# Kernel optimization log

Measured on AMD Instinct MI355X. Metric: run time of the kernel, lower is better.

Reference implementation:

```python
import jax, jax.numpy as jnp
import numpy as np

B, S, D, H = 4, 2048, 1024, 16
DH = D // H          # per-head attention size (attention_size // n_heads)
F = 4 * D            # FFN hidden
EPS = 1e-5


def _layer_norm(x, g, b):
    m = jnp.mean(x, axis=-1, keepdims=True)
    v = jnp.mean(jnp.square(x - m), axis=-1, keepdims=True)
    return (x - m) * jax.lax.rsqrt(v + EPS) * g + b


def setup_inputs() -> dict:
    key = jax.random.key(0)
    ks = jax.random.split(key, 12)
    s = 0.02
    x = jax.random.normal(ks[0], (B, S, D), dtype=jnp.float32)
    # causal mask: True = masked (strict upper triangle)
    mask = jnp.broadcast_to(jnp.triu(jnp.ones((S, S), dtype=bool), k=1), (B, S, S))
    wq = jax.random.normal(ks[1], (H, D, DH), dtype=jnp.float32) * s
    wk = jax.random.normal(ks[2], (H, D, DH), dtype=jnp.float32) * s
    wv = jax.random.normal(ks[3], (H, D, DH), dtype=jnp.float32) * s
    wo = jax.random.normal(ks[4], (D, D), dtype=jnp.float32) * s   # attention_size -> embedding_dim
    w1 = jax.random.normal(ks[5], (D, F), dtype=jnp.float32) * s
    b1 = jax.random.normal(ks[6], (F,), dtype=jnp.float32) * s
    w2 = jax.random.normal(ks[7], (F, D), dtype=jnp.float32) * s
    b2 = jax.random.normal(ks[8], (D,), dtype=jnp.float32) * s
    ln1_g = jnp.ones((D,), jnp.float32) + jax.random.normal(ks[9], (D,), jnp.float32) * s
    ln1_b = jax.random.normal(ks[10], (D,), jnp.float32) * s
    ln2_g = jnp.ones((D,), jnp.float32) + jax.random.normal(ks[11], (D,), jnp.float32) * s
    ln2_b = jnp.zeros((D,), jnp.float32)
    return {"x": x, "mask": mask, "wq": wq, "wk": wk, "wv": wv, "wo": wo,
            "w1": w1, "b1": b1, "w2": w2, "b2": b2,
            "ln1_g": ln1_g, "ln1_b": ln1_b, "ln2_g": ln2_g, "ln2_b": ln2_b}


def reference(x, mask, wq, wk, wv, wo, w1, b1, w2, b2, ln1_g, ln1_b, ln2_g, ln2_b):
    # --- self-attention block (pre-norm, residual) ---
    h = _layer_norm(x, ln1_g, ln1_b)                       # [B,S,D]
    q = jnp.einsum('bsd,hde->bhse', h, wq)                 # [B,H,S,DH]
    k = jnp.einsum('bsd,hde->bhse', h, wk)
    v = jnp.einsum('bsd,hde->bhse', h, wv)
    scores = jnp.einsum('bhse,bhte->bhst', q, k)           # [B,H,S,S]
    # faithful to source: mask-fill with -inf, THEN divide by sqrt(head_dim)
    scores = jnp.where(mask[:, None, :, :], -jnp.inf, scores) / jnp.sqrt(jnp.float32(DH))
    p = jax.nn.softmax(scores, axis=-1)
    attn = jnp.einsum('bhst,bhte->bhse', p, v)             # [B,H,S,DH]
    concat = attn.transpose(0, 2, 1, 3).reshape(B, S, D)   # heads concatenated on feature dim
    x = x + concat @ wo
    # --- feed-forward block ---
    h2 = _layer_norm(x, ln2_g, ln2_b)
    ff = jax.nn.gelu(h2 @ w1 + b1, approximate=False) @ w2 + b2
    return x + ff
```

## Files before the change

kernel.cpp:

```cpp
#include <hip/hip_runtime.h>
#include <hip/hip_bf16.h>
#include <math.h>


#define Bz 4
#define Sz 2048
#define Dz 1024
#define Hz 16
#define DHz 64
#define Fz 4096
#define Mz 8192

typedef float f32x4 __attribute__((ext_vector_type(4)));
typedef __bf16 bf16x8 __attribute__((ext_vector_type(8)));
typedef __bf16 bf16x4 __attribute__((ext_vector_type(4)));
typedef short s16x4 __attribute__((ext_vector_type(4)));

#define GLOAD_LDS16(g, l)                                                                   \
  __builtin_amdgcn_global_load_lds((const __attribute__((address_space(1))) unsigned int*)(g), \
                                   (__attribute__((address_space(3))) unsigned int*)(l), 16, 0, 0)

static __device__ __forceinline__ unsigned short f2bu(float f) {
  unsigned int u = __float_as_uint(f);
  u += 0x7fffu + ((u >> 16) & 1u);
  return (unsigned short)(u >> 16);
}

static __device__ __forceinline__ f32x4 mfma32(bf16x8 a, bf16x8 b, f32x4 c) {
  return __builtin_amdgcn_mfma_f32_16x16x32_bf16(a, b, c, 0, 0, 0);
}
static __device__ __forceinline__ f32x4 mfma16(s16x4 a, s16x4 b, f32x4 c) {
#if __has_builtin(__builtin_amdgcn_mfma_f32_16x16x16bf16_1k)
  return __builtin_amdgcn_mfma_f32_16x16x16bf16_1k(a, b, c, 0, 0, 0);
#else
  asm("v_mfma_f32_16x16x16_bf16 %0, %1, %2, %0" : "+v"(c) : "v"(a), "v"(b));
  return c;
#endif
}

template <int OFF>
static __device__ __forceinline__ s16x4 tr16(unsigned addr) {
  s16x4 r;
  asm volatile("ds_read_b64_tr_b16 %0, %1 offset:%2" : "=v"(r) : "v"(addr), "i"(OFF));
  return r;
}


__global__ __launch_bounds__(256) void pack_qkv(
    const float* __restrict__ wq, const float* __restrict__ wk, const float* __restrict__ wv,
    unsigned short* __restrict__ outW)
{
  __shared__ float tile[64][65];
  const int blk = blockIdx.x;
  const int dc = blk & 15;
  const int h  = (blk >> 4) & 15;
  const int p  = blk >> 8;
  const float* w = p == 0 ? wq : (p == 1 ? wk : wv);
  const int tid = threadIdx.x;
#pragma unroll
  for (int i = 0; i < 4; ++i) {
    int idx = i * 256 + tid;
    int dl = idx >> 4;
    int e0 = (idx & 15) * 4;
    const float4 v = *(const float4*)&w[(size_t)(h * 1024 + dc * 64 + dl) * 64 + e0];
    tile[dl][e0 + 0] = v.x; tile[dl][e0 + 1] = v.y;
    tile[dl][e0 + 2] = v.z; tile[dl][e0 + 3] = v.w;
  }
  __syncthreads();
#pragma unroll
  for (int i = 0; i < 4; ++i) {
    int idx = i * 256 + tid;
    int e = idx >> 4;
    int d0 = (idx & 15) * 4;
    ushort4 o;
    o.x = f2bu(tile[d0 + 0][e]); o.y = f2bu(tile[d0 + 1][e]);
    o.z = f2bu(tile[d0 + 2][e]); o.w = f2bu(tile[d0 + 3][e]);
    *(ushort4*)&outW[(size_t)(p * 1024 + h * 64 + e) * 1024 + dc * 64 + d0] = o;
  }
}

__global__ __launch_bounds__(256) void transpose_f32_to_bf16(
    const float* __restrict__ in, unsigned short* __restrict__ out, int R, int C)
{
  __shared__ float tile[32][33];
  int c0 = blockIdx.x * 32, r0 = blockIdx.y * 32;
  int x = threadIdx.x, y = threadIdx.y;
#pragma unroll
  for (int i = 0; i < 32; i += 8)
    tile[y + i][x] = in[(size_t)(r0 + y + i) * C + c0 + x];
  __syncthreads();
#pragma unroll
  for (int i = 0; i < 32; i += 8)
    out[(size_t)(c0 + y + i) * R + r0 + x] = f2bu(tile[x][y + i]);
}


__global__ __launch_bounds__(256) void ln_kernel(
    const float* __restrict__ x, const float* __restrict__ gamma, const float* __restrict__ beta,
    unsigned short* __restrict__ outH)
{
  const int row = blockIdx.x;
  const int tid = threadIdx.x;
  const float4 v = ((const float4*)(x + (size_t)row * Dz))[tid];
  float s = v.x + v.y + v.z + v.w;
  float s2 = v.x * v.x + v.y * v.y + v.z * v.z + v.w * v.w;
#pragma unroll
  for (int o = 32; o > 0; o >>= 1) {
    s += __shfl_xor(s, o);
    s2 += __shfl_xor(s2, o);
  }
  __shared__ float ss[4], ss2[4];
  if ((tid & 63) == 0) { ss[tid >> 6] = s; ss2[tid >> 6] = s2; }
  __syncthreads();
  s = ss[0] + ss[1] + ss[2] + ss[3];
  s2 = ss2[0] + ss2[1] + ss2[2] + ss2[3];
  const float mean = s * (1.0f / Dz);
  const float rstd = rsqrtf(s2 * (1.0f / Dz) - mean * mean + 1e-5f);
  const float4 g4 = ((const float4*)gamma)[tid];
  const float4 b4 = ((const float4*)beta)[tid];
  ushort4 o;
  o.x = f2bu((v.x - mean) * rstd * g4.x + b4.x);
  o.y = f2bu((v.y - mean) * rstd * g4.y + b4.y);
  o.z = f2bu((v.z - mean) * rstd * g4.z + b4.z);
  o.w = f2bu((v.w - mean) * rstd * g4.w + b4.w);
  ((ushort4*)(outH + (size_t)row * Dz))[tid] = o;
}


enum { EPI_BF16 = 0, EPI_GELU_BF16 = 1, EPI_RES_F32 = 2, EPI_BIAS_RES_F32 = 3 };

template <int BM, int EPI>
__global__ __launch_bounds__(512, 2) void gemm256(
    const unsigned short* __restrict__ A,
    const unsigned short* __restrict__ BT,
    int M, int N, int K,
    const float* bias, const float* resid,
    unsigned short* outb, float* outf)
{
  constexpr int BN = 256, BK = 32, DEPTH = 4;
  constexpr int ACH = BM / 128;
  constexpr int BCH = 2;
  constexpr int CH = ACH + BCH;
  constexpr int MREP = BM / 32;
  __shared__ unsigned short As[DEPTH][BM * BK];
  __shared__ unsigned short Bs[DEPTH][BN * BK];

  const int tid = threadIdx.x;
  const int lane = tid & 63;
  const int wid = tid >> 6;
  const int wr = wid >> 2;
  const int wc = wid & 3;
  const int rsel = lane & 15;
  const int kgrp = lane >> 4;

  const int nwg = gridDim.x;
  const int bid = blockIdx.x;
  const int id2 = (bid & 7) * (nwg >> 3) + (bid >> 3);
  const int nbx = N / BN;
  const int n0 = (id2 % nbx) * BN;
  const int m0 = (id2 / nbx) * BM;

  f32x4 acc[MREP][4] = {};

  auto issue = [&](int kt, int slot) {
#pragma unroll
    for (int r = 0; r < ACH; ++r) {
      int gc = r * 512 + tid;
      int row = gc >> 2;
      int kcs = (gc & 3) ^ ((row >> 1) & 3);
      GLOAD_LDS16(A + (size_t)(m0 + row) * K + kt * BK + kcs * 8, &As[slot][gc * 8]);
    }
#pragma unroll
    for (int r = 0; r < BCH; ++r) {
      int gc = r * 512 + tid;
      int row = gc >> 2;
      int kcs = (gc & 3) ^ ((row >> 1) & 3);
      GLOAD_LDS16(BT + (size_t)(n0 + row) * K + kt * BK + kcs * 8, &Bs[slot][gc * 8]);
    }
  };

  const int T = K >> 5;
  issue(0, 0); issue(1, 1); issue(2, 2);

  for (int t = 0; t < T; ++t) {
    const int slot = t & 3;
    if (t + 3 < T) issue(t + 3, (t + 3) & 3);
    int rem = T - 1 - t; if (rem > 3) rem = 3;
    if constexpr (CH == 4) {
      if (rem == 3)      asm volatile("s_waitcnt vmcnt(12)" ::: "memory");
      else if (rem == 2) asm volatile("s_waitcnt vmcnt(8)" ::: "memory");
      else if (rem == 1) asm volatile("s_waitcnt vmcnt(4)" ::: "memory");
      else               asm volatile("s_waitcnt vmcnt(0)" ::: "memory");
    } else {
      if (rem == 3)      asm volatile("s_waitcnt vmcnt(9)" ::: "memory");
      else if (rem == 2) asm volatile("s_waitcnt vmcnt(6)" ::: "memory");
      else if (rem == 1) asm volatile("s_waitcnt vmcnt(3)" ::: "memory");
      else               asm volatile("s_waitcnt vmcnt(0)" ::: "memory");
    }
    __builtin_amdgcn_sched_barrier(0);
    __builtin_amdgcn_s_barrier();
    __builtin_amdgcn_sched_barrier(0);

    const unsigned short* Ab = As[slot];
    const unsigned short* Bb = Bs[slot];
    __builtin_amdgcn_s_setprio(1);
    {
      bf16x8 bfr[4], af[MREP];
#pragma unroll
      for (int nf = 0; nf < 4; ++nf) {
        int br = wc * 64 + nf * 16 + rsel;
        bfr[nf] = *(const bf16x8*)&Bb[br * BK + ((kgrp ^ ((br >> 1) & 3)) * 8)];
      }
#pragma unroll
      for (int mf = 0; mf < MREP; ++mf) {
        int ar = wr * (BM / 2) + mf * 16 + rsel;
        af[mf] = *(const bf16x8*)&Ab[ar * BK + ((kgrp ^ ((ar >> 1) & 3)) * 8)];
      }
#pragma unroll
      for (int mf = 0; mf < MREP; ++mf)
#pragma unroll
        for (int nf = 0; nf < 4; ++nf)
          acc[mf][nf] = mfma32(af[mf], bfr[nf], acc[mf][nf]);
    }
    __builtin_amdgcn_s_setprio(0);
    __builtin_amdgcn_sched_barrier(0);
    __builtin_amdgcn_s_barrier();
  }

#pragma unroll
  for (int mf = 0; mf < MREP; ++mf) {
#pragma unroll
    for (int nf = 0; nf < 4; ++nf) {
      const int n = n0 + wc * 64 + nf * 16 + rsel;
#pragma unroll
      for (int j = 0; j < 4; ++j) {
        const int m = m0 + wr * (BM / 2) + mf * 16 + kgrp * 4 + j;
        const size_t idx = (size_t)m * N + n;
        float v = acc[mf][nf][j];
        if constexpr (EPI == EPI_BF16) {
          outb[idx] = f2bu(v);
        } else if constexpr (EPI == EPI_GELU_BF16) {
          v += bias[n];
          v = 0.5f * v * (1.0f + erff(v * 0.70710678118654752f));
          outb[idx] = f2bu(v);
        } else if constexpr (EPI == EPI_RES_F32) {
          outf[idx] = v + resid[idx];
        } else {
          outf[idx] = v + bias[n] + resid[idx];
        }
      }
    }
  }
}


__global__ __launch_bounds__(256, 4) void attn_kernel(
    const unsigned short* __restrict__ QKV,
    unsigned short* __restrict__ outA)
{
  __shared__ unsigned short Kt[64 * 64];
  __shared__ unsigned short Vs[64 * 64];
  const int pi = blockIdx.x;
  const int hh = blockIdx.y;
  const int bb = blockIdx.z;
  const int tid = threadIdx.x;
  const int lane = tid & 63;
  const int w = tid >> 6;
  const int rsel = lane & 15;
  const int kgrp = lane >> 4;
  const int qt[2] = {pi, 31 - pi};

  bf16x8 qf0[2], qf1[2];
  int qg[2];
#pragma unroll
  for (int s = 0; s < 2; ++s) {
    qg[s] = qt[s] * 64 + w * 16 + rsel;
    const size_t rowQ = (size_t)(bb * Sz + qg[s]) * 3072 + hh * 64;
    qf0[s] = *(const bf16x8*)&QKV[rowQ + kgrp * 8];
    qf1[s] = *(const bf16x8*)&QKV[rowQ + 32 + kgrp * 8];
  }

  f32x4 accO[2][4] = {};
  float mr[2] = {-INFINITY, -INFINITY};
  float lr[2] = {0.0f, 0.0f};

  auto vs3 = (__attribute__((address_space(3))) unsigned short*)Vs;
  const unsigned vbase = (unsigned)(uintptr_t)vs3 + (unsigned)lane * 8u;
  constexpr float SCL = 0.18033688011112042f;

  auto proc = [&](const bf16x8& q0, const bf16x8& q1, float& mrun, float& lrun,
                  f32x4* accS, s16x4* pb, bool edge, int qgs, int kb) {
    f32x4 sc[4];
    __builtin_amdgcn_s_setprio(1);
#pragma unroll
    for (int kf = 0; kf < 4; ++kf) {
      int key = kf * 16 + rsel;
      bf16x8 k0 = *(const bf16x8*)&Kt[key * 64 + ((kgrp ^ (key & 7)) * 8)];
      bf16x8 k1 = *(const bf16x8*)&Kt[key * 64 + (((4 + kgrp) ^ (key & 7)) * 8)];
      f32x4 s = {};
      s = mfma32(k0, q0, s);
      s = mfma32(k1, q1, s);
      sc[kf] = s;
    }
    __builtin_amdgcn_s_setprio(0);
    float tmax = -INFINITY;
#pragma unroll
    for (int kf = 0; kf < 4; ++kf)
#pragma unroll
      for (int j = 0; j < 4; ++j) {
        float v = sc[kf][j] * SCL;
        if (edge) {
          int keyg = kb + kf * 16 + kgrp * 4 + j;
          if (keyg > qgs) v = -INFINITY;
        }
        sc[kf][j] = v;
        tmax = fmaxf(tmax, v);
      }
    tmax = fmaxf(tmax, __shfl_xor(tmax, 16));
    tmax = fmaxf(tmax, __shfl_xor(tmax, 32));
    if (!__all(tmax <= mrun + 8.0f)) {
      const float mnew = fmaxf(mrun, tmax);
      const float corr = exp2f(mrun - mnew);
      lrun *= corr;
#pragma unroll
      for (int df = 0; df < 4; ++df) accS[df] *= corr;
      mrun = mnew;
    }
    float psum = 0.0f;
#pragma unroll
    for (int kf = 0; kf < 4; ++kf) {
      bf16x4 pv;
#pragma unroll
      for (int j = 0; j < 4; ++j) {
        float e = exp2f(sc[kf][j] - mrun);
        psum += e;
        pv[j] = (__bf16)e;
      }
      pb[kf] = __builtin_bit_cast(s16x4, pv);
    }
    psum += __shfl_xor(psum, 16);
    psum += __shfl_xor(psum, 32);
    lrun += psum;
  };

  for (int kt = 0; kt <= qt[1]; ++kt) {
    const int kb = kt * 64;
    if (kt) __syncthreads();
#pragma unroll
    for (int r = 0; r < 2; ++r) {
      int c = r * 256 + tid;
      int key = c >> 3;
      int dcs = (c & 7) ^ (key & 7);
      GLOAD_LDS16(QKV + (size_t)(bb * Sz + kb + key) * 3072 + 1024 + hh * 64 + dcs * 8,
                  &Kt[c * 8]);
    }
#pragma unroll
    for (int r = 0; r < 2; ++r) {
      int c = r * 256 + tid;
      int key = ((c >> 3) & 15) * 4 + ((c >> 1) & 3);
      int d = (c >> 7) * 16 + (c & 1) * 8;
      GLOAD_LDS16(QKV + (size_t)(bb * Sz + kb + key) * 3072 + 2048 + hh * 64 + d,
                  &Vs[c * 8]);
    }
    __syncthreads();

    s16x4 pb[2][4];
#pragma unroll
    for (int s = 0; s < 2; ++s)
      if (kt <= qt[s])
        proc(qf0[s], qf1[s], mr[s], lr[s], accO[s], pb[s], kt == qt[s], qg[s], kb);

#pragma unroll
    for (int df = 0; df < 4; ++df) {
      unsigned a = vbase + df * 2048;
      s16x4 vf0 = tr16<0>(a);
      s16x4 vf1 = tr16<512>(a);
      s16x4 vf2 = tr16<1024>(a);
      s16x4 vf3 = tr16<1536>(a);
      asm volatile("s_waitcnt lgkmcnt(0)" ::: "memory");
      __builtin_amdgcn_sched_barrier(0);
      __builtin_amdgcn_s_setprio(1);
#pragma unroll
      for (int s = 0; s < 2; ++s) {
        if (kt <= qt[s]) {
          accO[s][df] = mfma16(vf0, pb[s][0], accO[s][df]);
          accO[s][df] = mfma16(vf1, pb[s][1], accO[s][df]);
          accO[s][df] = mfma16(vf2, pb[s][2], accO[s][df]);
          accO[s][df] = mfma16(vf3, pb[s][3], accO[s][df]);
        }
      }
      __builtin_amdgcn_s_setprio(0);
    }
  }

#pragma unroll
  for (int s = 0; s < 2; ++s) {
    const float rl = 1.0f / lr[s];
    const size_t orow = (size_t)(bb * Sz + qg[s]) * Dz + hh * 64;
#pragma unroll
    for (int df = 0; df < 4; ++df) {
      s16x4 o;
#pragma unroll
      for (int j = 0; j < 4; ++j) o[j] = (short)f2bu(accO[s][df][j] * rl);
      *(s16x4*)&outA[orow + df * 16 + kgrp * 4] = o;
    }
  }
}


extern "C" void kernel_launch(void* const* d_in, const int* in_sizes, int n_in,
                              void* d_out, int out_size, void* d_ws, size_t ws_size,
                              hipStream_t stream) {
  const float* x   = (const float*)d_in[0];
  const float* wq  = (const float*)d_in[2];
  const float* wk  = (const float*)d_in[3];
  const float* wv  = (const float*)d_in[4];
  const float* wo  = (const float*)d_in[5];
  const float* w1  = (const float*)d_in[6];
  const float* b1  = (const float*)d_in[7];
  const float* w2  = (const float*)d_in[8];
  const float* b2  = (const float*)d_in[9];
  const float* g1  = (const float*)d_in[10];
  const float* be1 = (const float*)d_in[11];
  const float* g2  = (const float*)d_in[12];
  const float* be2 = (const float*)d_in[13];
  float* out = (float*)d_out;

  char* ws = (char*)d_ws;
  unsigned short* WqkvT = (unsigned short*)(ws);
  unsigned short* WoT   = (unsigned short*)(ws + 6291456);
  unsigned short* W1T   = (unsigned short*)(ws + 8388608);
  unsigned short* W2T   = (unsigned short*)(ws + 16777216);
  unsigned short* hbuf  = (unsigned short*)(ws + 25165824);
  unsigned short* big   = (unsigned short*)(ws + 41943040);

  dim3 tb(32, 8);
  pack_qkv<<<768, 256, 0, stream>>>(wq, wk, wv, WqkvT);
  transpose_f32_to_bf16<<<dim3(32, 32), tb, 0, stream>>>(wo, WoT, 1024, 1024);
  transpose_f32_to_bf16<<<dim3(128, 32), tb, 0, stream>>>(w1, W1T, 1024, 4096);
  transpose_f32_to_bf16<<<dim3(32, 128), tb, 0, stream>>>(w2, W2T, 4096, 1024);

  ln_kernel<<<Mz, 256, 0, stream>>>(x, g1, be1, hbuf);
  gemm256<128, EPI_BF16><<<768, 512, 0, stream>>>(
      hbuf, WqkvT, Mz, 3072, 1024, nullptr, nullptr, big, nullptr);
  attn_kernel<<<dim3(16, 16, 4), 256, 0, stream>>>(big, hbuf);
  gemm256<128, EPI_RES_F32><<<256, 512, 0, stream>>>(
      hbuf, WoT, Mz, 1024, 1024, nullptr, x, nullptr, out);
  ln_kernel<<<Mz, 256, 0, stream>>>(out, g2, be2, hbuf);
  gemm256<256, EPI_GELU_BF16><<<512, 512, 0, stream>>>(
      hbuf, W1T, Mz, Fz, 1024, b1, nullptr, big, nullptr);
  gemm256<128, EPI_BIAS_RES_F32><<<256, 512, 0, stream>>>(
      big, W2T, Mz, 1024, Fz, b2, out, nullptr, out);
}
```

Before: 497.0 us.

## Replace pipelined 256-wide GEMM with simple single-buffered 128x128 tile GEMM

Swaps the 512-thread, 4-stage multi-buffered GEMM for a 256-thread 128x128 tile kernel. The new kernel loads each K step into shared memory and waits before computing, with no prefetch overlap. The aim is to raise occupancy (3 blocks per CU) and spread work over more blocks, relying on parallelism to hide latency. In exchange it loses the overlap of loads with compute and gets less data reuse per tile.

```diff
diff --git a/kernel.cpp b/kernel.cpp
--- a/kernel.cpp
+++ b/kernel.cpp
@@ -129,112 +129,72 @@
 
 enum { EPI_BF16 = 0, EPI_GELU_BF16 = 1, EPI_RES_F32 = 2, EPI_BIAS_RES_F32 = 3 };
 
-template <int BM, int EPI>
-__global__ __launch_bounds__(512, 2) void gemm256(
+template <int EPI>
+__global__ __launch_bounds__(256, 3) void gemm128(
     const unsigned short* __restrict__ A,
     const unsigned short* __restrict__ BT,
     int M, int N, int K,
     const float* bias, const float* resid,
     unsigned short* outb, float* outf)
 {
-  constexpr int BN = 256, BK = 32, DEPTH = 4;
-  constexpr int ACH = BM / 128;
-  constexpr int BCH = 2;
-  constexpr int CH = ACH + BCH;
-  constexpr int MREP = BM / 32;
-  __shared__ unsigned short As[DEPTH][BM * BK];
-  __shared__ unsigned short Bs[DEPTH][BN * BK];
-
+  __shared__ unsigned short As[128 * 32];
+  __shared__ unsigned short Bs[128 * 32];
   const int tid = threadIdx.x;
   const int lane = tid & 63;
   const int wid = tid >> 6;
-  const int wr = wid >> 2;
-  const int wc = wid & 3;
+  const int wm = (wid >> 1) * 64;
+  const int wn = (wid & 1) * 64;
   const int rsel = lane & 15;
   const int kgrp = lane >> 4;
 
   const int nwg = gridDim.x;
   const int bid = blockIdx.x;
   const int id2 = (bid & 7) * (nwg >> 3) + (bid >> 3);
-  const int nbx = N / BN;
-  const int n0 = (id2 % nbx) * BN;
-  const int m0 = (id2 / nbx) * BM;
-
-  f32x4 acc[MREP][4] = {};
-
-  auto issue = [&](int kt, int slot) {
-#pragma unroll
-    for (int r = 0; r < ACH; ++r) {
-      int gc = r * 512 + tid;
+  const int nbx = N / 128;
+  const int n0 = (id2 % nbx) * 128;
+  const int m0 = (id2 / nbx) * 128;
+
+  f32x4 acc[4][4] = {};
+
+  const int T = K >> 5;
+  for (int t = 0; t < T; ++t) {
+    if (t) __syncthreads();
+    const int kOff = t * 32;
+#pragma unroll
+    for (int r = 0; r < 2; ++r) {
+      int gc = r * 256 + tid;
       int row = gc >> 2;
       int kcs = (gc & 3) ^ ((row >> 1) & 3);
-      GLOAD_LDS16(A + (size_t)(m0 + row) * K + kt * BK + kcs * 8, &As[slot][gc * 8]);
-    }
-#pragma unroll
-    for (int r = 0; r < BCH; ++r) {
-      int gc = r * 512 + tid;
-      int row = gc >> 2;
-      int kcs = (gc & 3) ^ ((row >> 1) & 3);
-      GLOAD_LDS16(BT + (size_t)(n0 + row) * K + kt * BK + kcs * 8, &Bs[slot][gc * 8]);
-    }
-  };
-
-  const int T = K >> 5;
-  issue(0, 0); issue(1, 1); issue(2, 2);
-
-  for (int t = 0; t < T; ++t) {
-    const int slot = t & 3;
-    if (t + 3 < T) issue(t + 3, (t + 3) & 3);
-    int rem = T - 1 - t; if (rem > 3) rem = 3;
-    if constexpr (CH == 4) {
-      if (rem == 3)      asm volatile("s_waitcnt vmcnt(12)" ::: "memory");
-      else if (rem == 2) asm volatile("s_waitcnt vmcnt(8)" ::: "memory");
-      else if (rem == 1) asm volatile("s_waitcnt vmcnt(4)" ::: "memory");
-      else               asm volatile("s_waitcnt vmcnt(0)" ::: "memory");
-    } else {
-      if (rem == 3)      asm volatile("s_waitcnt vmcnt(9)" ::: "memory");
-      else if (rem == 2) asm volatile("s_waitcnt vmcnt(6)" ::: "memory");
-      else if (rem == 1) asm volatile("s_waitcnt vmcnt(3)" ::: "memory");
-      else               asm volatile("s_waitcnt vmcnt(0)" ::: "memory");
-    }
-    __builtin_amdgcn_sched_barrier(0);
-    __builtin_amdgcn_s_barrier();
-    __builtin_amdgcn_sched_barrier(0);
-
-    const unsigned short* Ab = As[slot];
-    const unsigned short* Bb = Bs[slot];
-    __builtin_amdgcn_s_setprio(1);
-    {
-      bf16x8 bfr[4], af[MREP];
-#pragma unroll
-      for (int nf = 0; nf < 4; ++nf) {
-        int br = wc * 64 + nf * 16 + rsel;
-        bfr[nf] = *(const bf16x8*)&Bb[br * BK + ((kgrp ^ ((br >> 1) & 3)) * 8)];
-      }
-#pragma unroll
-      for (int mf = 0; mf < MREP; ++mf) {
-        int ar = wr * (BM / 2) + mf * 16 + rsel;
-        af[mf] = *(const bf16x8*)&Ab[ar * BK + ((kgrp ^ ((ar >> 1) & 3)) * 8)];
-      }
-#pragma unroll
-      for (int mf = 0; mf < MREP; ++mf)
-#pragma unroll
-        for (int nf = 0; nf < 4; ++nf)
-          acc[mf][nf] = mfma32(af[mf], bfr[nf], acc[mf][nf]);
-    }
-    __builtin_amdgcn_s_setprio(0);
-    __builtin_amdgcn_sched_barrier(0);
-    __builtin_amdgcn_s_barrier();
-  }
-
-#pragma unroll
-  for (int mf = 0; mf < MREP; ++mf) {
+      GLOAD_LDS16(A + (size_t)(m0 + row) * K + kOff + kcs * 8, &As[gc * 8]);
+      GLOAD_LDS16(BT + (size_t)(n0 + row) * K + kOff + kcs * 8, &Bs[gc * 8]);
+    }
+    __syncthreads();
+    bf16x8 af[4], bfr[4];
+#pragma unroll
+    for (int mf = 0; mf < 4; ++mf) {
+      int ar = wm + mf * 16 + rsel;
+      af[mf] = *(const bf16x8*)&As[ar * 32 + ((kgrp ^ ((ar >> 1) & 3)) * 8)];
+    }
 #pragma unroll
     for (int nf = 0; nf < 4; ++nf) {
-      const int n = n0 + wc * 64 + nf * 16 + rsel;
+      int br = wn + nf * 16 + rsel;
+      bfr[nf] = *(const bf16x8*)&Bs[br * 32 + ((kgrp ^ ((br >> 1) & 3)) * 8)];
+    }
+#pragma unroll
+    for (int mf = 0; mf < 4; ++mf)
+#pragma unroll
+      for (int nf = 0; nf < 4; ++nf)
+        acc[mf][nf] = mfma32(af[mf], bfr[nf], acc[mf][nf]);
+  }
+
+#pragma unroll
+  for (int mf = 0; mf < 4; ++mf) {
+#pragma unroll
+    for (int nf = 0; nf < 4; ++nf) {
+      const int n = n0 + wn + nf * 16 + rsel;
 #pragma unroll
       for (int j = 0; j < 4; ++j) {
-        const int m = m0 + wr * (BM / 2) + mf * 16 + kgrp * 4 + j;
+        const int m = m0 + wm + mf * 16 + kgrp * 4 + j;
         const size_t idx = (size_t)m * N + n;
         float v = acc[mf][nf][j];
         if constexpr (EPI == EPI_BF16) {
@@ -441,14 +401,14 @@
   transpose_f32_to_bf16<<<dim3(32, 128), tb, 0, stream>>>(w2, W2T, 4096, 1024);
 
   ln_kernel<<<Mz, 256, 0, stream>>>(x, g1, be1, hbuf);
-  gemm256<128, EPI_BF16><<<768, 512, 0, stream>>>(
+  gemm128<EPI_BF16><<<1536, 256, 0, stream>>>(
       hbuf, WqkvT, Mz, 3072, 1024, nullptr, nullptr, big, nullptr);
   attn_kernel<<<dim3(16, 16, 4), 256, 0, stream>>>(big, hbuf);
-  gemm256<128, EPI_RES_F32><<<256, 512, 0, stream>>>(
+  gemm128<EPI_RES_F32><<<512, 256, 0, stream>>>(
       hbuf, WoT, Mz, 1024, 1024, nullptr, x, nullptr, out);
   ln_kernel<<<Mz, 256, 0, stream>>>(out, g2, be2, hbuf);
-  gemm256<256, EPI_GELU_BF16><<<512, 512, 0, stream>>>(
+  gemm128<EPI_GELU_BF16><<<2048, 256, 0, stream>>>(
       hbuf, W1T, Mz, Fz, 1024, b1, nullptr, big, nullptr);
-  gemm256<128, EPI_BIAS_RES_F32><<<256, 512, 0, stream>>>(
+  gemm128<EPI_BIAS_RES_F32><<<512, 256, 0, stream>>>(
       big, W2T, Mz, 1024, Fz, b2, out, nullptr, out);
 }
```

Measured after the change: 429.8 us. 13.5% less time.
